# Kernel tuning notes

Measured on AMD Instinct MI355X. Metric: run time of the kernel, lower is better.

Reference implementation:

```python
import jax, jax.numpy as jnp
import numpy as np

B, S, D = 2, 400, 512  # batch, seq (src == tgt for self-attention), dim; attn_hidden=0 so d == D


def setup_inputs() -> dict:
    key = jax.random.key(0)
    ks = jax.random.split(key, 9)
    inv = 1.0 / np.sqrt(D)
    return {
        "input": jax.random.normal(ks[0], (B, S, D), jnp.float32),
        "memory_bank": jax.random.normal(ks[1], (B, S, D), jnp.float32),
        # lengths in [S//2, S], guaranteed >= 2 so no row is fully masked
        "memory_lengths": jax.random.randint(ks[2], (B,), S // 2, S + 1, jnp.int32),
        "Wq": jax.random.normal(ks[3], (D, D), jnp.float32) * inv,   # linear_query.weight^T
        "bq": jax.random.normal(ks[4], (D,), jnp.float32) * inv,      # linear_query.bias
        "Wc": jax.random.normal(ks[5], (D, D), jnp.float32) * inv,   # linear_context.weight^T
        "v": jax.random.normal(ks[6], (D,), jnp.float32) * inv,       # v.weight (d -> 1)
        "Wout": jax.random.normal(ks[7], (2 * D, D), jnp.float32) * inv,  # linear_out.weight^T
        "bout": jax.random.normal(ks[8], (D,), jnp.float32) * inv,
    }


def reference(input, memory_bank, memory_lengths, Wq, bq, Wc, v, Wout, bout):
    b, s, d = memory_bank.shape
    # Bahdanau/mlp score: v^T tanh(Wq q + b + Wc h)
    wq = jnp.einsum("btd,de->bte", input, Wq) + bq            # [B,T,d]
    uh = jnp.einsum("bsd,de->bse", memory_bank, Wc)           # [B,S,d]
    wquh = jnp.tanh(wq[:, :, None, :] + uh[:, None, :, :])    # [B,T,S,d] big intermediate
    scores = jnp.einsum("btse,e->bts", wquh, v)               # [B,T,S]
    # padding mask (j < length) with self position masked out on the diagonal
    pos = jnp.arange(s)
    key_mask = pos[None, :] < memory_lengths[:, None]         # [B,S]
    mask = key_mask[:, None, :] & (pos[:, None] != pos[None, :])  # [B,T,S]
    scores = jnp.where(mask, scores, -jnp.inf)
    align = jax.nn.softmax(scores, axis=2)                    # [B,T,S]
    c = jnp.einsum("bts,bsd->btd", align, memory_bank)        # context [B,T,D]
    concat_c = jnp.concatenate([c, input], axis=2)            # [B,T,2D]
    attn_h = jnp.einsum("btf,fd->btd", concat_c, Wout) + bout # [B,T,D]
    # mlp variant: no sigmoid gating
    return attn_h.transpose(1, 0, 2), align.transpose(1, 0, 2)  # [T,B,D], [T,B,S]
```

## Files before the change

### kernel.cpp

```cpp
#include <hip/hip_runtime.h>
#include <math.h>

#define BB 2
#define SS 400
#define DD 512
#define TWO_LOG2E 2.8853900817779268f

#if __has_builtin(__builtin_amdgcn_exp2f)
#define EXP2F(x) __builtin_amdgcn_exp2f(x)
#else
#define EXP2F(x) exp2f(x)
#endif
#define RCPF(x) __builtin_amdgcn_rcpf(x)

#define EAOFF 0
#define MOFF 409600
#define EB4OFF 819200
#define XOFF 1228800

typedef __bf16 bf16x8 __attribute__((ext_vector_type(8)));
typedef float floatx16 __attribute__((ext_vector_type(16)));

__global__ __launch_bounds__(256) void k0_all(
    const float* __restrict__ Wq, const float* __restrict__ Wc,
    const float* __restrict__ Wout, const float* __restrict__ input,
    const float* __restrict__ mbk, unsigned short* __restrict__ wt,
    unsigned short* __restrict__ ahi, unsigned short* __restrict__ alo)
{
    const int gid = blockIdx.x;
    if (gid < 1024) {
        const int g   = gid >> 9;
        const int rem = gid & 511;
        const int k0  = (rem & 15) * 32;
        const int n0  = (rem >> 4) * 32;

        __shared__ float tile[32][33];
        const int nn  = threadIdx.x & 31;
        const int kk0 = threadIdx.x >> 5;
        const int n   = n0 + nn;

        #pragma unroll
        for (int p = 0; p < 4; ++p) {
            const int k = k0 + kk0 + p * 8;
            float val;
            if (n0 < 512) val = (g ? Wc : Wq)[(size_t)k * 512 + n];
            else          val = Wout[((size_t)(g ? k : 512 + k)) * 512 + (n - 512)];
            tile[kk0 + p * 8][nn] = val;
        }
        __syncthreads();

        const int kc = threadIdx.x & 31;
        #pragma unroll
        for (int p = 0; p < 4; ++p) {
            const int nl = (threadIdx.x >> 5) + p * 8;
            const __bf16 h = (__bf16)tile[kc][nl];
            wt[((size_t)(g * 1024 + n0 + nl)) * 512 + k0 + kc] =
                __builtin_bit_cast(unsigned short, h);
        }
    } else {
        const int cid = gid - 1024;
        const int g   = (cid >= 400) ? 1 : 0;
        const int i4  = (cid - g * 400) * 256 + threadIdx.x;
        const float4 a = ((const float4*)(g ? mbk : input))[i4];
        ushort4 h, l;
        #pragma unroll
        for (int j = 0; j < 4; ++j) {
            const float av = (&a.x)[j];
            const __bf16 hh = (__bf16)av;
            (&h.x)[j] = __builtin_bit_cast(unsigned short, hh);
            const __bf16 ll = (__bf16)(av - (float)hh);
            (&l.x)[j] = __builtin_bit_cast(unsigned short, ll);
        }
        ((ushort4*)(ahi + (size_t)g * 409600))[i4] = h;
        ((ushort4*)(alo + (size_t)g * 409600))[i4] = l;
    }
}

__global__ __launch_bounds__(64) void k1_mfma(
    const unsigned short* __restrict__ ahi, const unsigned short* __restrict__ alo,
    const unsigned short* __restrict__ wt, const float* __restrict__ bq,
    const float* __restrict__ bout, float* __restrict__ ws,
    float* __restrict__ out0)
{
    const int lane = threadIdx.x;
    const int mt   = blockIdx.x;
    const int np   = blockIdx.y;
    const int g    = blockIdx.z;
    const int m    = lane & 31;
    const int kh   = lane >> 5;
    const int n0   = np * 64;

    const size_t arow = ((size_t)g * 800 + mt * 32 + m) * 512 + kh * 8;
    const unsigned short* __restrict__ ah = ahi + arow;
    const unsigned short* __restrict__ al = alo + arow;
    const unsigned short* __restrict__ w0 =
        wt + ((size_t)(g * 1024 + n0 + m)) * 512 + kh * 8;
    const unsigned short* __restrict__ w1 = w0 + (size_t)32 * 512;

    floatx16 acc0h, acc0l, acc1h, acc1l;
    #pragma unroll
    for (int i = 0; i < 16; ++i) { acc0h[i] = 0.f; acc0l[i] = 0.f;
                                   acc1h[i] = 0.f; acc1l[i] = 0.f; }

    #pragma unroll 4
    for (int ks = 0; ks < 32; ++ks) {
        const bf16x8 va0 = *(const bf16x8*)(ah + ks * 16);
        const bf16x8 va1 = *(const bf16x8*)(al + ks * 16);
        const bf16x8 bh0 = *(const bf16x8*)(w0 + ks * 16);
        const bf16x8 bh1 = *(const bf16x8*)(w1 + ks * 16);

        acc0h = __builtin_amdgcn_mfma_f32_32x32x16_bf16(va0, bh0, acc0h, 0, 0, 0);
        acc0l = __builtin_amdgcn_mfma_f32_32x32x16_bf16(va1, bh0, acc0l, 0, 0, 0);
        acc1h = __builtin_amdgcn_mfma_f32_32x32x16_bf16(va0, bh1, acc1h, 0, 0, 0);
        acc1l = __builtin_amdgcn_mfma_f32_32x32x16_bf16(va1, bh1, acc1l, 0, 0, 0);
    }

    const floatx16 c0 = acc0h + acc0l;
    const floatx16 c1 = acc1h + acc1l;
    const int rbase = kh * 4;

    #pragma unroll
    for (int r = 0; r < 16; ++r) {
        const int row  = (r & 3) + 8 * (r >> 2) + rbase;
        const int grow = mt * 32 + row;
        const int bi   = (grow >= SS) ? 1 : 0;
        const int rl   = grow - bi * SS;
        #pragma unroll
        for (int u = 0; u < 2; ++u) {
            const float val  = u ? c1[r] : c0[r];
            const int   gcol = n0 + u * 32 + m;
            if (g == 0) {
                if (gcol < 512) {
                    ws[EAOFF + (size_t)grow * 512 + gcol] =
                        EXP2F(TWO_LOG2E * (val + bq[gcol]));
                } else {
                    const int d = gcol - 512;
                    out0[((size_t)(rl * BB + bi)) * 512 + d] = val + bout[d];
                }
            } else {
                if (gcol < 512) {
                    ws[EB4OFF + (size_t)((bi * 128 + (gcol >> 2)) * SS + rl) * 4
                       + (gcol & 3)] = EXP2F(TWO_LOG2E * val);
                } else {
                    ws[MOFF + (size_t)grow * 512 + (gcol - 512)] = val;
                }
            }
        }
    }
}

__global__ __launch_bounds__(1024, 8) void k2_attn(
    const float* __restrict__ ws, const float* __restrict__ v,
    const int* __restrict__ lens, float* __restrict__ out1,
    float* __restrict__ out0)
{
    const int tp  = blockIdx.x;
    const int b   = blockIdx.y;
    const int t0  = tp * 2;
    const int tid = threadIdx.x;
    const int th  = tid >> 9;
    const int s   = tid & 511;
    const int t   = t0 + th;
    const int sidx = (s < SS) ? s : 0;
    const int len  = lens[b];

    __shared__ float lea[2][512];
    __shared__ float lv[512];
    __shared__ float lal[SS][2];
    __shared__ float wredm[16], wreds[16];

    if (th == 0) lv[s] = v[s];
    lea[th][s] = ws[EAOFF + (size_t)(b * SS + t) * 512 + s];
    __syncthreads();

    const float4* __restrict__ eb4 =
        (const float4*)(ws + EB4OFF) + (size_t)b * 128 * SS + sidx;

    float a0 = 0.f, a1 = 0.f, a2 = 0.f, a3 = 0.f;
    #pragma unroll 4
    for (int e4 = 0; e4 < 128; ++e4) {
        const float4 eb = eb4[(size_t)e4 * SS];
        const float4 vv = *(const float4*)&lv[e4 * 4];
        const float4 ea = *(const float4*)&lea[th][e4 * 4];
        a0 = fmaf(vv.x, RCPF(fmaf(ea.x, eb.x, 1.f)), a0);
        a1 = fmaf(vv.y, RCPF(fmaf(ea.y, eb.y, 1.f)), a1);
        a2 = fmaf(vv.z, RCPF(fmaf(ea.z, eb.z, 1.f)), a2);
        a3 = fmaf(vv.w, RCPF(fmaf(ea.w, eb.w, 1.f)), a3);
    }
    const float acc = (a0 + a1) + (a2 + a3);

    const bool ok = (s < SS) && (s < len) && (s != t);
    const float sc = ok ? -2.f * acc : -INFINITY;

    const int wid  = tid >> 6;
    const int lane = tid & 63;

    float m = sc;
    #pragma unroll
    for (int off = 32; off > 0; off >>= 1)
        m = fmaxf(m, __shfl_xor(m, off));
    if (lane == 0) wredm[wid] = m;
    __syncthreads();
    float mx = wredm[th * 8];
    #pragma unroll
    for (int w = 1; w < 8; ++w) mx = fmaxf(mx, wredm[th * 8 + w]);

    const float p = ok ? __expf(sc - mx) : 0.f;
    float sv = p;
    #pragma unroll
    for (int off = 32; off > 0; off >>= 1)
        sv += __shfl_xor(sv, off);
    if (lane == 0) wreds[wid] = sv;
    __syncthreads();
    float tot = wreds[th * 8];
    #pragma unroll
    for (int w = 1; w < 8; ++w) tot += wreds[th * 8 + w];
    const float inv = RCPF(tot);

    if (s < SS) {
        const float al = p * inv;
        out1[((size_t)(t * BB) + b) * SS + s] = al;
        lal[s][th] = al;
    }
    __syncthreads();

    const float* __restrict__ Mb = ws + MOFF + (size_t)b * SS * DD;
    const int d = s;
    float c0 = 0.f, c1 = 0.f, c2 = 0.f, c3 = 0.f;
    #pragma unroll 4
    for (int sp = 0; sp < SS; sp += 4) {
        c0 = fmaf(lal[sp    ][th], Mb[(size_t)(sp    ) * DD + d], c0);
        c1 = fmaf(lal[sp + 1][th], Mb[(size_t)(sp + 1) * DD + d], c1);
        c2 = fmaf(lal[sp + 2][th], Mb[(size_t)(sp + 2) * DD + d], c2);
        c3 = fmaf(lal[sp + 3][th], Mb[(size_t)(sp + 3) * DD + d], c3);
    }
    out0[((size_t)(t * BB) + b) * DD + d] += (c0 + c1) + (c2 + c3);
}

extern "C" void kernel_launch(void* const* d_in, const int* in_sizes, int n_in,
                              void* d_out, int out_size, void* d_ws, size_t ws_size,
                              hipStream_t stream)
{
    const float* input = (const float*)d_in[0];
    const float* mbk   = (const float*)d_in[1];
    const int*   lens  = (const int*)d_in[2];
    const float* Wq    = (const float*)d_in[3];
    const float* bq    = (const float*)d_in[4];
    const float* Wc    = (const float*)d_in[5];
    const float* v     = (const float*)d_in[6];
    const float* Wout  = (const float*)d_in[7];
    const float* bout  = (const float*)d_in[8];

    float* out0 = (float*)d_out;
    float* out1 = out0 + (size_t)BB * SS * DD;
    float* ws   = (float*)d_ws;
    unsigned short* x16 = (unsigned short*)(ws + XOFF);
    unsigned short* wt  = x16;
    unsigned short* ahi = x16 + 1048576;
    unsigned short* alo = ahi + 819200;

    hipLaunchKernelGGL(k0_all, dim3(1824), dim3(256), 0, stream,
                       Wq, Wc, Wout, input, mbk, wt, ahi, alo);
    hipLaunchKernelGGL(k1_mfma, dim3(25, 16, 2), dim3(64), 0, stream,
                       ahi, alo, wt, bq, bout, ws, out0);
    hipLaunchKernelGGL(k2_attn, dim3(200, 2), dim3(1024), 0, stream,
                       ws, v, lens, out1, out0);
}
```

Baseline: 159.6 us.

## Process four queries per thread and combine four reciprocals into one

The attention kernel now assigns four query rows to each 512-thread block instead of two rows per 1024-thread block. Each thread reuses one load of the precomputed key exponentials across all four queries, and the context pass reuses each memory-bank value for four rows. Inside the score loop the four reciprocal terms per float4 are merged into a single fraction, leaving one rcp and extra multiplies. This cuts global and shared traffic and transcendental work per score, but halves the block count to 200 and adds register pressure, and the merged fraction may lose some precision.

After: 156.5 us. 1.02x faster.

```diff
diff --git a/kernel.cpp b/kernel.cpp
--- a/kernel.cpp
+++ b/kernel.cpp
@@ -149,92 +149,140 @@
     }
 }
 
-__global__ __launch_bounds__(1024, 8) void k2_attn(
+__global__ __launch_bounds__(512) void k2_attn(
     const float* __restrict__ ws, const float* __restrict__ v,
     const int* __restrict__ lens, float* __restrict__ out1,
     float* __restrict__ out0)
 {
-    const int tp  = blockIdx.x;
-    const int b   = blockIdx.y;
-    const int t0  = tp * 2;
+    const int tq = blockIdx.x;
+    const int b  = blockIdx.y;
+    const int t0 = tq * 4;
     const int tid = threadIdx.x;
-    const int th  = tid >> 9;
-    const int s   = tid & 511;
-    const int t   = t0 + th;
+    const int s   = tid;
     const int sidx = (s < SS) ? s : 0;
     const int len  = lens[b];
 
-    __shared__ float lea[2][512];
+    __shared__ float lea[4][512];
     __shared__ float lv[512];
-    __shared__ float lal[SS][2];
-    __shared__ float wredm[16], wreds[16];
-
-    if (th == 0) lv[s] = v[s];
-    lea[th][s] = ws[EAOFF + (size_t)(b * SS + t) * 512 + s];
+    __shared__ float4 lal4[SS];
+    __shared__ float wredm[4][8], wreds[4][8];
+
+    lv[tid] = v[tid];
+    #pragma unroll
+    for (int j = 0; j < 4; ++j)
+        lea[j][tid] = ws[EAOFF + (size_t)(b * SS + t0 + j) * 512 + tid];
     __syncthreads();
 
     const float4* __restrict__ eb4 =
         (const float4*)(ws + EB4OFF) + (size_t)b * 128 * SS + sidx;
 
-    float a0 = 0.f, a1 = 0.f, a2 = 0.f, a3 = 0.f;
+    float acc[4] = {0.f, 0.f, 0.f, 0.f};
     #pragma unroll 4
     for (int e4 = 0; e4 < 128; ++e4) {
         const float4 eb = eb4[(size_t)e4 * SS];
         const float4 vv = *(const float4*)&lv[e4 * 4];
-        const float4 ea = *(const float4*)&lea[th][e4 * 4];
-        a0 = fmaf(vv.x, RCPF(fmaf(ea.x, eb.x, 1.f)), a0);
-        a1 = fmaf(vv.y, RCPF(fmaf(ea.y, eb.y, 1.f)), a1);
-        a2 = fmaf(vv.z, RCPF(fmaf(ea.z, eb.z, 1.f)), a2);
-        a3 = fmaf(vv.w, RCPF(fmaf(ea.w, eb.w, 1.f)), a3);
-    }
-    const float acc = (a0 + a1) + (a2 + a3);
-
-    const bool ok = (s < SS) && (s < len) && (s != t);
-    const float sc = ok ? -2.f * acc : -INFINITY;
+        #pragma unroll
+        for (int j = 0; j < 4; ++j) {
+            const float4 ea = *(const float4*)&lea[j][e4 * 4];
+            const float d0 = fmaf(ea.x, eb.x, 1.f);
+            const float d1 = fmaf(ea.y, eb.y, 1.f);
+            const float d2 = fmaf(ea.z, eb.z, 1.f);
+            const float d3 = fmaf(ea.w, eb.w, 1.f);
+            const float d01 = d0 * d1, d23 = d2 * d3;
+            const float n01 = fmaf(vv.x, d1, vv.y * d0);
+            const float n23 = fmaf(vv.z, d3, vv.w * d2);
+            const float num = fmaf(n01, d23, n23 * d01);
+            acc[j] = fmaf(num, RCPF(d01 * d23), acc[j]);
+        }
+    }
 
     const int wid  = tid >> 6;
     const int lane = tid & 63;
 
-    float m = sc;
-    #pragma unroll
-    for (int off = 32; off > 0; off >>= 1)
-        m = fmaxf(m, __shfl_xor(m, off));
-    if (lane == 0) wredm[wid] = m;
-    __syncthreads();
-    float mx = wredm[th * 8];
-    #pragma unroll
-    for (int w = 1; w < 8; ++w) mx = fmaxf(mx, wredm[th * 8 + w]);
-
-    const float p = ok ? __expf(sc - mx) : 0.f;
-    float sv = p;
-    #pragma unroll
-    for (int off = 32; off > 0; off >>= 1)
-        sv += __shfl_xor(sv, off);
-    if (lane == 0) wreds[wid] = sv;
-    __syncthreads();
-    float tot = wreds[th * 8];
-    #pragma unroll
-    for (int w = 1; w < 8; ++w) tot += wreds[th * 8 + w];
-    const float inv = RCPF(tot);
+    bool  ok[4];
+    float sc[4];
+    #pragma unroll
+    for (int j = 0; j < 4; ++j) {
+        ok[j] = (s < SS) && (s < len) && (s != t0 + j);
+        sc[j] = ok[j] ? -2.f * acc[j] : -INFINITY;
+    }
+
+    float m[4] = {sc[0], sc[1], sc[2], sc[3]};
+    #pragma unroll
+    for (int off = 32; off > 0; off >>= 1) {
+        #pragma unroll
+        for (int j = 0; j < 4; ++j)
+            m[j] = fmaxf(m[j], __shfl_xor(m[j], off));
+    }
+    if (lane == 0) {
+        #pragma unroll
+        for (int j = 0; j < 4; ++j) wredm[j][wid] = m[j];
+    }
+    __syncthreads();
+    float mx[4];
+    #pragma unroll
+    for (int j = 0; j < 4; ++j) {
+        mx[j] = wredm[j][0];
+        #pragma unroll
+        for (int w = 1; w < 8; ++w) mx[j] = fmaxf(mx[j], wredm[j][w]);
+    }
+    __syncthreads();
+
+    float p[4];
+    #pragma unroll
+    for (int j = 0; j < 4; ++j)
+        p[j] = ok[j] ? __expf(sc[j] - mx[j]) : 0.f;
+    float sv[4] = {p[0], p[1], p[2], p[3]};
+    #pragma unroll
+    for (int off = 32; off > 0; off >>= 1) {
+        #pragma unroll
+        for (int j = 0; j < 4; ++j)
+            sv[j] += __shfl_xor(sv[j], off);
+    }
+    if (lane == 0) {
+        #pragma unroll
+        for (int j = 0; j < 4; ++j) wreds[j][wid] = sv[j];
+    }
+    __syncthreads();
+    float inv[4];
+    #pragma unroll
+    for (int j = 0; j < 4; ++j) {
+        float tot = wreds[j][0];
+        #pragma unroll
+        for (int w = 1; w < 8; ++w) tot += wreds[j][w];
+        inv[j] = RCPF(tot);
+    }
 
     if (s < SS) {
-        const float al = p * inv;
-        out1[((size_t)(t * BB) + b) * SS + s] = al;
-        lal[s][th] = al;
+        float4 al;
+        al.x = p[0] * inv[0];
+        al.y = p[1] * inv[1];
+        al.z = p[2] * inv[2];
+        al.w = p[3] * inv[3];
+        out1[((size_t)((t0 + 0) * BB) + b) * SS + s] = al.x;
+        out1[((size_t)((t0 + 1) * BB) + b) * SS + s] = al.y;
+        out1[((size_t)((t0 + 2) * BB) + b) * SS + s] = al.z;
+        out1[((size_t)((t0 + 3) * BB) + b) * SS + s] = al.w;
+        lal4[s] = al;
     }
     __syncthreads();
 
     const float* __restrict__ Mb = ws + MOFF + (size_t)b * SS * DD;
-    const int d = s;
+    const int d = tid;
     float c0 = 0.f, c1 = 0.f, c2 = 0.f, c3 = 0.f;
-    #pragma unroll 4
-    for (int sp = 0; sp < SS; sp += 4) {
-        c0 = fmaf(lal[sp    ][th], Mb[(size_t)(sp    ) * DD + d], c0);
-        c1 = fmaf(lal[sp + 1][th], Mb[(size_t)(sp + 1) * DD + d], c1);
-        c2 = fmaf(lal[sp + 2][th], Mb[(size_t)(sp + 2) * DD + d], c2);
-        c3 = fmaf(lal[sp + 3][th], Mb[(size_t)(sp + 3) * DD + d], c3);
-    }
-    out0[((size_t)(t * BB) + b) * DD + d] += (c0 + c1) + (c2 + c3);
+    #pragma unroll 8
+    for (int sp = 0; sp < SS; ++sp) {
+        const float  mv = Mb[(size_t)sp * DD + d];
+        const float4 la = lal4[sp];
+        c0 = fmaf(la.x, mv, c0);
+        c1 = fmaf(la.y, mv, c1);
+        c2 = fmaf(la.z, mv, c2);
+        c3 = fmaf(la.w, mv, c3);
+    }
+    out0[((size_t)((t0 + 0) * BB) + b) * DD + d] += c0;
+    out0[((size_t)((t0 + 1) * BB) + b) * DD + d] += c1;
+    out0[((size_t)((t0 + 2) * BB) + b) * DD + d] += c2;
+    out0[((size_t)((t0 + 3) * BB) + b) * DD + d] += c3;
 }
 
 extern "C" void kernel_launch(void* const* d_in, const int* in_sizes, int n_in,
@@ -263,6 +311,6 @@
                        Wq, Wc, Wout, input, mbk, wt, ahi, alo);
     hipLaunchKernelGGL(k1_mfma, dim3(25, 16, 2), dim3(64), 0, stream,
                        ahi, alo, wt, bq, bout, ws, out0);
-    hipLaunchKernelGGL(k2_attn, dim3(200, 2), dim3(1024), 0, stream,
+    hipLaunchKernelGGL(k2_attn, dim3(100, 2), dim3(512), 0, stream,
                        ws, v, lens, out1, out0);
 }
```
